# Optimization experiments

Hardware: AMD Instinct MI355X
Metric: run time of the kernel (lower is better)

The kernel has to match this reference:

```python
import jax, jax.numpy as jnp
import numpy as np
import math

HIDDEN_SIZE = 1024

def setup_inputs() -> dict:
    key = jax.random.key(0)
    hidden_states = jax.random.normal(key, (64, 4096, HIDDEN_SIZE), dtype=jnp.float32)
    return {"hidden_states": hidden_states}

def reference(hidden_states) -> jnp.ndarray:
    # hidden_states: [B, S, H]; query is last timestep, attends over all S keys.
    scale = math.sqrt(HIDDEN_SIZE)
    query = hidden_states[:, -1, :]                          # [B, H]
    scores = jnp.einsum('bh,bsh->bs', query, hidden_states) / scale  # [B, S]
    weights = jax.nn.softmax(scores, axis=-1)                # [B, S]
    attended = jnp.einsum('bs,bsh->bh', weights, hidden_states)      # [B, H]
    return attended
```

## Files before the change

kernel.cpp:

```cpp
#include <hip/hip_runtime.h>


#define B 64
#define S 4096
#define H 1024
#define NCHUNK 32
#define ROWS_PER_BLOCK (S / NCHUNK)

__global__ __launch_bounds__(256) void attn_partial(
    const float* __restrict__ hs,
    float* __restrict__ acc,
    float* __restrict__ lsum)
{
    const int tid  = threadIdx.x;
    const int lane = tid & 63;
    const int wave = tid >> 6;
    const int chunk = blockIdx.x;
    const int b     = blockIdx.y;

    const float4* qrow = (const float4*)(hs + ((size_t)b * S + (S - 1)) * H);
    const float4 q0 = qrow[lane];
    const float4 q1 = qrow[lane + 64];
    const float4 q2 = qrow[lane + 128];
    const float4 q3 = qrow[lane + 192];

    float4 a0 = {0.f,0.f,0.f,0.f}, a1 = {0.f,0.f,0.f,0.f};
    float4 a2 = {0.f,0.f,0.f,0.f}, a3 = {0.f,0.f,0.f,0.f};
    float l = 0.f;

    const int s0 = chunk * ROWS_PER_BLOCK + wave;
    #pragma unroll 2
    for (int i = 0; i < ROWS_PER_BLOCK / 4; ++i) {
        const int s = s0 + i * 4;
        const float4* row = (const float4*)(hs + ((size_t)b * S + s) * H);
        const float4 h0 = row[lane];
        const float4 h1 = row[lane + 64];
        const float4 h2 = row[lane + 128];
        const float4 h3 = row[lane + 192];

        float p = h0.x*q0.x + h0.y*q0.y + h0.z*q0.z + h0.w*q0.w
                + h1.x*q1.x + h1.y*q1.y + h1.z*q1.z + h1.w*q1.w
                + h2.x*q2.x + h2.y*q2.y + h2.z*q2.z + h2.w*q2.w
                + h3.x*q3.x + h3.y*q3.y + h3.z*q3.z + h3.w*q3.w;

        #pragma unroll
        for (int off = 32; off > 0; off >>= 1)
            p += __shfl_xor(p, off, 64);

        const float w = __expf(p * 0.03125f);
        l += w;
        a0.x += w * h0.x; a0.y += w * h0.y; a0.z += w * h0.z; a0.w += w * h0.w;
        a1.x += w * h1.x; a1.y += w * h1.y; a1.z += w * h1.z; a1.w += w * h1.w;
        a2.x += w * h2.x; a2.y += w * h2.y; a2.z += w * h2.z; a2.w += w * h2.w;
        a3.x += w * h3.x; a3.y += w * h3.y; a3.z += w * h3.z; a3.w += w * h3.w;
    }

    __shared__ float sacc[4][H];
    __shared__ float sl[4];
    float4* sa = (float4*)sacc[wave];
    sa[lane]       = a0;
    sa[lane + 64]  = a1;
    sa[lane + 128] = a2;
    sa[lane + 192] = a3;
    if (lane == 0) sl[wave] = l;
    __syncthreads();

    const float4 v0 = ((const float4*)sacc[0])[tid];
    const float4 v1 = ((const float4*)sacc[1])[tid];
    const float4 v2 = ((const float4*)sacc[2])[tid];
    const float4 v3 = ((const float4*)sacc[3])[tid];
    float* accb = acc + (size_t)b * H + tid * 4;
    atomicAdd(accb + 0, v0.x + v1.x + v2.x + v3.x);
    atomicAdd(accb + 1, v0.y + v1.y + v2.y + v3.y);
    atomicAdd(accb + 2, v0.z + v1.z + v2.z + v3.z);
    atomicAdd(accb + 3, v0.w + v1.w + v2.w + v3.w);
    if (tid == 0) atomicAdd(lsum + b, sl[0] + sl[1] + sl[2] + sl[3]);
}

__global__ __launch_bounds__(256) void attn_norm(
    const float* __restrict__ acc,
    const float* __restrict__ lsum,
    float* __restrict__ out)
{
    const int b = blockIdx.x;
    const float inv = 1.0f / lsum[b];
    float4 v = ((const float4*)(acc + (size_t)b * H))[threadIdx.x];
    v.x *= inv; v.y *= inv; v.z *= inv; v.w *= inv;
    ((float4*)(out + (size_t)b * H))[threadIdx.x] = v;
}

extern "C" void kernel_launch(void* const* d_in, const int* in_sizes, int n_in,
                              void* d_out, int out_size, void* d_ws, size_t ws_size,
                              hipStream_t stream) {
    const float* hs = (const float*)d_in[0];
    float* out  = (float*)d_out;
    float* acc  = (float*)d_ws;
    float* lsum = acc + (size_t)B * H;

    hipMemsetAsync(d_ws, 0, ((size_t)B * H + B) * sizeof(float), stream);
    attn_partial<<<dim3(NCHUNK, B), 256, 0, stream>>>(hs, acc, lsum);
    attn_norm<<<B, 256, 0, stream>>>(acc, lsum, out);
}
```

Measured before the change: 1.319 ms.

## Process two rows per iteration and replace atomics with per-chunk partials plus reduce

The main loop now loads two rows per wave iteration, computing both dot products and interleaving their shuffle reductions to expose more memory-level parallelism. Global float atomics and the workspace memset are replaced by per-chunk partial writes (B*NCHUNK*H floats) and a second kernel that sums the 32 partials and normalizes. This removes atomic contention and one launch, at the cost of extra register pressure and about 8 MB of partial traffic.

Result: no change. 1.328 ms (+0.7%).

```diff
diff --git a/kernel.cpp b/kernel.cpp
--- a/kernel.cpp
+++ b/kernel.cpp
@@ -9,8 +9,8 @@
 
 __global__ __launch_bounds__(256) void attn_partial(
     const float* __restrict__ hs,
-    float* __restrict__ acc,
-    float* __restrict__ lsum)
+    float* __restrict__ pacc,
+    float* __restrict__ pl)
 {
     const int tid  = threadIdx.x;
     const int lane = tid & 63;
@@ -30,29 +30,44 @@
 
     const int s0 = chunk * ROWS_PER_BLOCK + wave;
     #pragma unroll 2
-    for (int i = 0; i < ROWS_PER_BLOCK / 4; ++i) {
-        const int s = s0 + i * 4;
-        const float4* row = (const float4*)(hs + ((size_t)b * S + s) * H);
-        const float4 h0 = row[lane];
-        const float4 h1 = row[lane + 64];
-        const float4 h2 = row[lane + 128];
-        const float4 h3 = row[lane + 192];
+    for (int i = 0; i < ROWS_PER_BLOCK / 8; ++i) {
+        const float4* rowA = (const float4*)(hs + ((size_t)b * S + s0 + i*8    ) * H);
+        const float4* rowB = (const float4*)(hs + ((size_t)b * S + s0 + i*8 + 4) * H);
+        const float4 hA0 = rowA[lane];
+        const float4 hA1 = rowA[lane + 64];
+        const float4 hA2 = rowA[lane + 128];
+        const float4 hA3 = rowA[lane + 192];
+        const float4 hB0 = rowB[lane];
+        const float4 hB1 = rowB[lane + 64];
+        const float4 hB2 = rowB[lane + 128];
+        const float4 hB3 = rowB[lane + 192];
 
-        float p = h0.x*q0.x + h0.y*q0.y + h0.z*q0.z + h0.w*q0.w
-                + h1.x*q1.x + h1.y*q1.y + h1.z*q1.z + h1.w*q1.w
-                + h2.x*q2.x + h2.y*q2.y + h2.z*q2.z + h2.w*q2.w
-                + h3.x*q3.x + h3.y*q3.y + h3.z*q3.z + h3.w*q3.w;
+        float pA = hA0.x*q0.x + hA0.y*q0.y + hA0.z*q0.z + hA0.w*q0.w
+                 + hA1.x*q1.x + hA1.y*q1.y + hA1.z*q1.z + hA1.w*q1.w
+                 + hA2.x*q2.x + hA2.y*q2.y + hA2.z*q2.z + hA2.w*q2.w
+                 + hA3.x*q3.x + hA3.y*q3.y + hA3.z*q3.z + hA3.w*q3.w;
+        float pB = hB0.x*q0.x + hB0.y*q0.y + hB0.z*q0.z + hB0.w*q0.w
+                 + hB1.x*q1.x + hB1.y*q1.y + hB1.z*q1.z + hB1.w*q1.w
+                 + hB2.x*q2.x + hB2.y*q2.y + hB2.z*q2.z + hB2.w*q2.w
+                 + hB3.x*q3.x + hB3.y*q3.y + hB3.z*q3.z + hB3.w*q3.w;
 
         #pragma unroll
-        for (int off = 32; off > 0; off >>= 1)
-            p += __shfl_xor(p, off, 64);
+        for (int off = 32; off > 0; off >>= 1) {
+            pA += __shfl_xor(pA, off, 64);
+            pB += __shfl_xor(pB, off, 64);
+        }
 
-        const float w = __expf(p * 0.03125f);
-        l += w;
-        a0.x += w * h0.x; a0.y += w * h0.y; a0.z += w * h0.z; a0.w += w * h0.w;
-        a1.x += w * h1.x; a1.y += w * h1.y; a1.z += w * h1.z; a1.w += w * h1.w;
-        a2.x += w * h2.x; a2.y += w * h2.y; a2.z += w * h2.z; a2.w += w * h2.w;
-        a3.x += w * h3.x; a3.y += w * h3.y; a3.z += w * h3.z; a3.w += w * h3.w;
+        const float wA = __expf(pA * 0.03125f);
+        const float wB = __expf(pB * 0.03125f);
+        l += wA + wB;
+        a0.x += wA*hA0.x + wB*hB0.x; a0.y += wA*hA0.y + wB*hB0.y;
+        a0.z += wA*hA0.z + wB*hB0.z; a0.w += wA*hA0.w + wB*hB0.w;
+        a1.x += wA*hA1.x + wB*hB1.x; a1.y += wA*hA1.y + wB*hB1.y;
+        a1.z += wA*hA1.z + wB*hB1.z; a1.w += wA*hA1.w + wB*hB1.w;
+        a2.x += wA*hA2.x + wB*hB2.x; a2.y += wA*hA2.y + wB*hB2.y;
+        a2.z += wA*hA2.z + wB*hB2.z; a2.w += wA*hA2.w + wB*hB2.w;
+        a3.x += wA*hA3.x + wB*hB3.x; a3.y += wA*hA3.y + wB*hB3.y;
+        a3.z += wA*hA3.z + wB*hB3.z; a3.w += wA*hA3.w + wB*hB3.w;
     }
 
     __shared__ float sacc[4][H];
@@ -69,24 +84,36 @@
     const float4 v1 = ((const float4*)sacc[1])[tid];
     const float4 v2 = ((const float4*)sacc[2])[tid];
     const float4 v3 = ((const float4*)sacc[3])[tid];
-    float* accb = acc + (size_t)b * H + tid * 4;
-    atomicAdd(accb + 0, v0.x + v1.x + v2.x + v3.x);
-    atomicAdd(accb + 1, v0.y + v1.y + v2.y + v3.y);
-    atomicAdd(accb + 2, v0.z + v1.z + v2.z + v3.z);
-    atomicAdd(accb + 3, v0.w + v1.w + v2.w + v3.w);
-    if (tid == 0) atomicAdd(lsum + b, sl[0] + sl[1] + sl[2] + sl[3]);
+    float4 v;
+    v.x = v0.x + v1.x + v2.x + v3.x;
+    v.y = v0.y + v1.y + v2.y + v3.y;
+    v.z = v0.z + v1.z + v2.z + v3.z;
+    v.w = v0.w + v1.w + v2.w + v3.w;
+    ((float4*)(pacc + ((size_t)b * NCHUNK + chunk) * H))[tid] = v;
+    if (tid == 0) pl[b * NCHUNK + chunk] = sl[0] + sl[1] + sl[2] + sl[3];
 }
 
-__global__ __launch_bounds__(256) void attn_norm(
-    const float* __restrict__ acc,
-    const float* __restrict__ lsum,
+__global__ __launch_bounds__(256) void attn_reduce(
+    const float* __restrict__ pacc,
+    const float* __restrict__ pl,
     float* __restrict__ out)
 {
     const int b = blockIdx.x;
-    const float inv = 1.0f / lsum[b];
-    float4 v = ((const float4*)(acc + (size_t)b * H))[threadIdx.x];
+    const int tid = threadIdx.x;
+
+    float l = 0.f;
+    #pragma unroll
+    for (int c = 0; c < NCHUNK; ++c) l += pl[b * NCHUNK + c];
+
+    float4 v = {0.f, 0.f, 0.f, 0.f};
+    #pragma unroll 4
+    for (int c = 0; c < NCHUNK; ++c) {
+        const float4 p = ((const float4*)(pacc + ((size_t)b * NCHUNK + c) * H))[tid];
+        v.x += p.x; v.y += p.y; v.z += p.z; v.w += p.w;
+    }
+    const float inv = 1.0f / l;
     v.x *= inv; v.y *= inv; v.z *= inv; v.w *= inv;
-    ((float4*)(out + (size_t)b * H))[threadIdx.x] = v;
+    ((float4*)(out + (size_t)b * H))[tid] = v;
 }
 
 extern "C" void kernel_launch(void* const* d_in, const int* in_sizes, int n_in,
@@ -94,10 +121,9 @@
                               hipStream_t stream) {
     const float* hs = (const float*)d_in[0];
     float* out  = (float*)d_out;
-    float* acc  = (float*)d_ws;
-    float* lsum = acc + (size_t)B * H;
+    float* pacc = (float*)d_ws;
+    float* pl   = pacc + (size_t)B * NCHUNK * H;
 
-    hipMemsetAsync(d_ws, 0, ((size_t)B * H + B) * sizeof(float), stream);
-    attn_partial<<<dim3(NCHUNK, B), 256, 0, stream>>>(hs, acc, lsum);
-    attn_norm<<<B, 256, 0, stream>>>(acc, lsum, out);
+    attn_partial<<<dim3(NCHUNK, B), 256, 0, stream>>>(hs, pacc, pl);
+    attn_reduce<<<B, 256, 0, stream>>>(pacc, pl, out);
 }
```
